# Optimization experiments

Hardware: AMD Instinct MI355X
Metric: run time of the kernel (lower is better)

## Reference

```python
import jax, jax.numpy as jnp
import numpy as np

B, P, C, T, V, H, A = 256, 620, 512, 32, 140, 256, 256


def setup_inputs() -> dict:
    key = jax.random.key(0)
    ks = jax.random.split(key, 8)
    s = lambda k, shape, sc: (jax.random.normal(k, shape, jnp.float32) * sc)
    return {
        "img_features": jax.random.normal(ks[0], (B, P, C), jnp.float32),
        "targets": jax.random.normal(ks[1], (B, T, V), jnp.float32),
        "Ic_w": s(ks[2], (A, C), 0.02), "Ic_b": jnp.zeros((A,), jnp.float32),
        "Hc_w": s(ks[3], (A, H), 0.02), "Hc_b": jnp.zeros((A,), jnp.float32),
        "W_ih": s(ks[4], (4 * H, V + A), 0.02), "W_hh": s(ks[5], (4 * H, H), 0.02),
        "b_ih": jnp.zeros((4 * H,), jnp.float32), "b_hh": jnp.zeros((4 * H,), jnp.float32),
        "Cd_w": s(ks[6], (V, H), 0.02), "Cd_b": jnp.zeros((V,), jnp.float32),
    }


def reference(img_features, targets, Ic_w, Ic_b, Hc_w, Hc_b,
              W_ih, W_hh, b_ih, b_hh, Cd_w, Cd_b):
    # Project image features once: attn_img = Ic(img_features)  [B,P,A]
    attn_img = jnp.einsum('bpc,ac->bpa', img_features, Ic_w) + Ic_b
    scale = 1.0 / jnp.sqrt(jnp.float32(A))
    h0 = jnp.zeros((B, H), jnp.float32)
    c0 = jnp.zeros((B, H), jnp.float32)
    x0 = targets[:, 0, :]  # <start> token logits/one-hot, fed as first rnn input

    def step(carry, _):
        h, c, x = carry
        # attn_hidden = Hc(hidden): [B,A]
        q = h @ Hc_w.T + Hc_b
        # scaled dot-product attention over pixels (keys=values=attn_img)
        w = jax.nn.softmax(jnp.einsum('ba,bpa->bp', q, attn_img) * scale, axis=-1)
        ctx = jnp.einsum('bp,bpa->ba', w, attn_img)  # [B,A]
        # single-step LSTM (PyTorch gate order: i, f, g, o)
        inp = jnp.concatenate([x, ctx], axis=-1)  # [B, V+A]
        gates = inp @ W_ih.T + b_ih + h @ W_hh.T + b_hh
        i, f, g, o = jnp.split(gates, 4, axis=-1)
        c2 = jax.nn.sigmoid(f) * c + jax.nn.sigmoid(i) * jnp.tanh(g)
        h2 = jax.nn.sigmoid(o) * jnp.tanh(c2)
        out = h2 @ Cd_w.T + Cd_b  # [B,V] vocab logits
        # eval path: next rnn_input is the predicted logits
        return (h2, c2, out), out

    _, outs = jax.lax.scan(step, (h0, c0, x0), None, length=T)
    return jnp.transpose(outs, (1, 0, 2))  # [B,T,V]
```

## Files before the change

### kernel.cpp

```cpp
#include <hip/hip_runtime.h>
#include <stdint.h>

#define B_ 256
#define P_ 620
#define C_ 512
#define T_ 32
#define V_ 140
#define H_ 256
#define A_ 256
#define KC 672
#define LOG2E 1.4426950408889634f

typedef unsigned short u16;
typedef __attribute__((ext_vector_type(8))) short bf16x8;
typedef __attribute__((ext_vector_type(4))) float f32x4;

__device__ __forceinline__ float bf2f(u16 u) {
  union { unsigned int i; float f; } v; v.i = ((unsigned int)u) << 16; return v.f;
}
__device__ __forceinline__ float bfu_lo(unsigned int u) {
  union { unsigned int i; float f; } v; v.i = u << 16; return v.f;
}
__device__ __forceinline__ float bfu_hi(unsigned int u) {
  union { unsigned int i; float f; } v; v.i = u & 0xffff0000u; return v.f;
}
__device__ __forceinline__ u16 f2bf(float f) {
  union { float f; unsigned int i; } v; v.f = f;
  unsigned int x = v.i;
  return (u16)((x + 0x7fffu + ((x >> 16) & 1u)) >> 16);
}
__device__ __forceinline__ float sigf(float x) {
  return 1.f / (1.f + __builtin_exp2f(-x * LOG2E));
}
__device__ __forceinline__ float tanhfast(float x) {
  return 1.f - 2.f / (__builtin_exp2f(2.f * LOG2E * x) + 1.f);
}
__device__ __forceinline__ float ld_any(const void* p, size_t idx, int f32) {
  return f32 ? ((const float*)p)[idx] : bf2f(((const u16*)p)[idx]);
}
__device__ __forceinline__ bf16x8 ld8_any(const void* base, size_t off, int f32) {
  if (f32) {
    const float4* p = (const float4*)((const float*)base + off);
    float4 x = p[0], y = p[1];
    bf16x8 r;
    r[0] = (short)f2bf(x.x); r[1] = (short)f2bf(x.y);
    r[2] = (short)f2bf(x.z); r[3] = (short)f2bf(x.w);
    r[4] = (short)f2bf(y.x); r[5] = (short)f2bf(y.y);
    r[6] = (short)f2bf(y.z); r[7] = (short)f2bf(y.w);
    return r;
  }
  return *(const bf16x8*)((const u16*)base + off);
}
__device__ __forceinline__ float dot8(uint4 u, float4 iA, float4 iB) {
  return bfu_lo(u.x) * iA.x + bfu_hi(u.x) * iA.y
       + bfu_lo(u.y) * iA.z + bfu_hi(u.y) * iA.w
       + bfu_lo(u.z) * iB.x + bfu_hi(u.z) * iB.y
       + bfu_lo(u.w) * iB.z + bfu_hi(u.w) * iB.w;
}

__global__ void k_detect(const unsigned int* __restrict__ img, int* __restrict__ flag) {
  __shared__ int mx[256];
  unsigned int u = img[threadIdx.x];
  mx[threadIdx.x] = (int)((u >> 7) & 0xffu);
  __syncthreads();
  if (threadIdx.x == 0) {
    int m = 0;
    #pragma unroll 16
    for (int i = 0; i < 256; i++) m = (mx[i] > m) ? mx[i] : m;
    *flag = (m >= 0x90) ? 1 : 0;
  }
}

__global__ void k_init(const void* __restrict__ W_ih, const void* __restrict__ W_hh,
                       const void* __restrict__ b_ih, const void* __restrict__ b_hh,
                       const void* __restrict__ Hc_w, const void* __restrict__ Hc_b,
                       const void* __restrict__ Cd_w, const void* __restrict__ Cd_b,
                       u16* __restrict__ W_t, float* __restrict__ bias_cat,
                       u16* __restrict__ Hc_wb, float* __restrict__ hcb_f,
                       u16* __restrict__ Cd_wb, float* __restrict__ cdb_f,
                       const int* __restrict__ flag) {
  const int f32 = *flag;
  const int tid = blockIdx.x * blockDim.x + threadIdx.x;
  const int nthr = gridDim.x * blockDim.x;
  for (int idx = tid; idx < 1024 * KC; idx += nthr) {
    int jq = idx / KC, k = idx - jq * KC;
    int j = jq >> 2, q = jq & 3, n = q * H_ + j;
    u16 v = 0;
    if (k < 396) v = f2bf(ld_any(W_ih, (size_t)n * 396 + k, f32));
    else if (k < 652) v = f2bf(ld_any(W_hh, (size_t)n * H_ + (k - 396), f32));
    W_t[(size_t)(k >> 3) * 8192 + jq * 8 + (k & 7)] = v;
  }
  for (int n = tid; n < 1024; n += nthr) {
    int j = n >> 2, q = n & 3, on = q * H_ + j;
    bias_cat[n] = ld_any(b_ih, on, f32) + ld_any(b_hh, on, f32);
  }
  for (int idx = tid; idx < H_ * A_; idx += nthr) Hc_wb[idx] = f2bf(ld_any(Hc_w, idx, f32));
  for (int idx = tid; idx < V_ * H_; idx += nthr) Cd_wb[idx] = f2bf(ld_any(Cd_w, idx, f32));
  for (int n = tid; n < A_; n += nthr) hcb_f[n] = ld_any(Hc_b, n, f32);
  for (int n = tid; n < V_; n += nthr) cdb_f[n] = ld_any(Cd_b, n, f32);
}

__global__ __launch_bounds__(256) void k_proj(const void* __restrict__ img,
                                              const void* __restrict__ Ic_w,
                                              const void* __restrict__ Ic_b,
                                              u16* __restrict__ attn_img,
                                              const int* __restrict__ flag) {
  __shared__ __align__(16) short As[128 * 32];
  __shared__ __align__(16) short Bs[128 * 32];
  const int f32 = *flag;
  const int tid = threadIdx.x;
  const int lane = tid & 63, w = tid >> 6;
  const int wg = blockIdx.x;
  const int m0 = ((wg & 7) + (wg >> 4) * 8) * 128;
  const int n0 = ((wg >> 3) & 1) * 128;
  f32x4 acc[4][4] = {};
  const int wm = w & 1, wn = w >> 1;
  const int fr = lane & 15, fq = lane >> 4;
  const int srow = tid >> 2, scol = (tid & 3) * 8;
  for (int kt = 0; kt < C_; kt += 32) {
    bf16x8 a0 = ld8_any(img, (size_t)(m0 + srow) * C_ + kt + scol, f32);
    bf16x8 a1 = ld8_any(img, (size_t)(m0 + srow + 64) * C_ + kt + scol, f32);
    bf16x8 b0 = ld8_any(Ic_w, (size_t)(n0 + srow) * C_ + kt + scol, f32);
    bf16x8 b1 = ld8_any(Ic_w, (size_t)(n0 + srow + 64) * C_ + kt + scol, f32);
    __syncthreads();
    *(bf16x8*)(As + tid * 8) = a0;
    *(bf16x8*)(As + (tid + 256) * 8) = a1;
    *(bf16x8*)(Bs + tid * 8) = b0;
    *(bf16x8*)(Bs + (tid + 256) * 8) = b1;
    __syncthreads();
    bf16x8 af[4], bfr[4];
    #pragma unroll
    for (int i = 0; i < 4; i++)
      af[i] = *(const bf16x8*)(As + (wm * 64 + i * 16 + fr) * 32 + fq * 8);
    #pragma unroll
    for (int j = 0; j < 4; j++)
      bfr[j] = *(const bf16x8*)(Bs + (wn * 64 + j * 16 + fr) * 32 + fq * 8);
    #pragma unroll
    for (int i = 0; i < 4; i++)
      #pragma unroll
      for (int j = 0; j < 4; j++)
        acc[i][j] = __builtin_amdgcn_mfma_f32_16x16x32_bf16(af[i], bfr[j], acc[i][j], 0, 0, 0);
  }
  #pragma unroll
  for (int i = 0; i < 4; i++) {
    #pragma unroll
    for (int j = 0; j < 4; j++) {
      const int col = n0 + wn * 64 + j * 16 + fr;
      const float bias = ld_any(Ic_b, col, f32);
      #pragma unroll
      for (int rr = 0; rr < 4; rr++) {
        const int row = m0 + wm * 64 + i * 16 + fq * 4 + rr;
        attn_img[(size_t)row * A_ + col] = f2bf(acc[i][j][rr] + bias);
      }
    }
  }
}

__global__ __launch_bounds__(512) void k_seq(
    const u16* __restrict__ Hc_wb, const float* __restrict__ hcb_f,
    const u16* __restrict__ Cd_wb, const float* __restrict__ cdb_f,
    const u16* __restrict__ W_t, const float* __restrict__ bias_cat,
    const u16* __restrict__ attn_img, const void* __restrict__ targets,
    void* __restrict__ d_out, const int* __restrict__ flag) {
  __shared__ float h_s[H_];
  __shared__ float q_s[A_];
  __shared__ __align__(16) float inp_s[KC];
  __shared__ __align__(16) float ctx_s[4][A_];
  __shared__ float red_l[4];
  __shared__ __align__(16) float gpart[1024];
  const int f32 = *flag;
  const int b = blockIdx.x;
  const int tid = threadIdx.x;
  const int lane = tid & 63, w = tid >> 6;

  if (tid < H_) h_s[tid] = 0.f;
  for (int i = tid; i < KC; i += 512) inp_s[i] = 0.f;
  if (tid < V_) inp_s[tid] = ld_any(targets, (size_t)b * T_ * V_ + tid, f32);
  float c_reg = 0.f;
  float4 bias4 = make_float4(0.f, 0.f, 0.f, 0.f);
  if (tid >= 256) bias4 = *(const float4*)(bias_cat + 4 * (tid - 256));
  const float sc = 0.0625f * LOG2E;
  __syncthreads();

  for (int t = 0; t < T_; t++) {
    if (tid < A_) {
      float acc = hcb_f[tid];
      const uint2* wr = (const uint2*)(Hc_wb + tid * H_);
      #pragma unroll 8
      for (int j = 0; j < H_ / 4; j++) {
        uint2 u = wr[j];
        acc += bfu_lo(u.x) * h_s[4 * j] + bfu_hi(u.x) * h_s[4 * j + 1]
             + bfu_lo(u.y) * h_s[4 * j + 2] + bfu_hi(u.y) * h_s[4 * j + 3];
      }
      q_s[tid] = acc;
    } else if (t > 0 && tid < A_ + V_) {
      const int v = tid - A_;
      float acc = cdb_f[v];
      const uint2* wr = (const uint2*)(Cd_wb + v * H_);
      #pragma unroll 8
      for (int j = 0; j < H_ / 4; j++) {
        uint2 u = wr[j];
        acc += bfu_lo(u.x) * h_s[4 * j] + bfu_hi(u.x) * h_s[4 * j + 1]
             + bfu_lo(u.y) * h_s[4 * j + 2] + bfu_hi(u.y) * h_s[4 * j + 3];
      }
      const size_t oo = (size_t)b * T_ * V_ + (size_t)(t - 1) * V_ + v;
      if (f32) ((float*)d_out)[oo] = acc;
      else ((u16*)d_out)[oo] = f2bf(acc);
      inp_s[v] = acc;
    }
    __syncthreads();

    if (w < 4) {
      const int l16 = lane & 15, g = lane >> 4;
      float qr[16];
      #pragma unroll
      for (int e = 0; e < 8; e++) {
        qr[e] = q_s[l16 * 8 + e];
        qr[8 + e] = q_s[128 + l16 * 8 + e];
      }
      const uint4* ap = (const uint4*)(attn_img + (size_t)b * P_ * A_);
      const int pbase = w * 4 + g;
      float l_acc = 0.f;
      float cx[16] = {};
      #pragma unroll 3
      for (int it = 0; it < 39; it++) {
        const int p = pbase + it * 16;
        const int pc = (p < P_) ? p : (P_ - 1);
        const uint4 u0 = ap[(size_t)pc * 32 + l16];
        const uint4 u1 = ap[(size_t)pc * 32 + 16 + l16];
        float v[16];
        v[0] = bfu_lo(u0.x); v[1] = bfu_hi(u0.x);
        v[2] = bfu_lo(u0.y); v[3] = bfu_hi(u0.y);
        v[4] = bfu_lo(u0.z); v[5] = bfu_hi(u0.z);
        v[6] = bfu_lo(u0.w); v[7] = bfu_hi(u0.w);
        v[8] = bfu_lo(u1.x); v[9] = bfu_hi(u1.x);
        v[10] = bfu_lo(u1.y); v[11] = bfu_hi(u1.y);
        v[12] = bfu_lo(u1.z); v[13] = bfu_hi(u1.z);
        v[14] = bfu_lo(u1.w); v[15] = bfu_hi(u1.w);
        float s0 = qr[0] * v[0] + qr[1] * v[1] + qr[2] * v[2] + qr[3] * v[3];
        float s1 = qr[4] * v[4] + qr[5] * v[5] + qr[6] * v[6] + qr[7] * v[7];
        float s2 = qr[8] * v[8] + qr[9] * v[9] + qr[10] * v[10] + qr[11] * v[11];
        float s3 = qr[12] * v[12] + qr[13] * v[13] + qr[14] * v[14] + qr[15] * v[15];
        float s = (s0 + s1) + (s2 + s3);
        s += __shfl_xor(s, 1); s += __shfl_xor(s, 2);
        s += __shfl_xor(s, 4); s += __shfl_xor(s, 8);
        const float sl = (p < P_) ? s * sc : -3.0e38f;
        const float es = __builtin_exp2f(sl - 16.f);
        l_acc += es;
        #pragma unroll
        for (int k = 0; k < 16; k++) cx[k] += es * v[k];
      }
      #pragma unroll
      for (int k = 0; k < 16; k++) {
        cx[k] += __shfl_xor(cx[k], 16);
        cx[k] += __shfl_xor(cx[k], 32);
      }
      l_acc += __shfl_xor(l_acc, 16);
      l_acc += __shfl_xor(l_acc, 32);
      if (g == 0) {
        #pragma unroll
        for (int e = 0; e < 8; e++) {
          ctx_s[w][l16 * 8 + e] = cx[e];
          ctx_s[w][128 + l16 * 8 + e] = cx[8 + e];
        }
        if (l16 == 0) red_l[w] = l_acc;
      }
    } else {
      const int r = tid - 256;
      const uint4* wt4 = (const uint4*)W_t + 4 * r;
      float g0 = bias4.x, g1 = bias4.y, g2 = bias4.z, g3 = bias4.w;
      #pragma unroll 2
      for (int kk = 0; kk < 17; kk++) {
        const float4 iA = *(const float4*)(inp_s + kk * 8);
        const float4 iB = *(const float4*)(inp_s + kk * 8 + 4);
        const uint4 u0 = wt4[kk * 1024 + 0];
        const uint4 u1 = wt4[kk * 1024 + 1];
        const uint4 u2 = wt4[kk * 1024 + 2];
        const uint4 u3 = wt4[kk * 1024 + 3];
        g0 += dot8(u0, iA, iB); g1 += dot8(u1, iA, iB);
        g2 += dot8(u2, iA, iB); g3 += dot8(u3, iA, iB);
      }
      #pragma unroll 2
      for (int kk = 50; kk < 84; kk++) {
        const float4 iA = *(const float4*)(inp_s + kk * 8);
        const float4 iB = *(const float4*)(inp_s + kk * 8 + 4);
        const uint4 u0 = wt4[kk * 1024 + 0];
        const uint4 u1 = wt4[kk * 1024 + 1];
        const uint4 u2 = wt4[kk * 1024 + 2];
        const uint4 u3 = wt4[kk * 1024 + 3];
        g0 += dot8(u0, iA, iB); g1 += dot8(u1, iA, iB);
        g2 += dot8(u2, iA, iB); g3 += dot8(u3, iA, iB);
      }
      gpart[4 * r + 0] = g0; gpart[4 * r + 1] = g1;
      gpart[4 * r + 2] = g2; gpart[4 * r + 3] = g3;
    }
    __syncthreads();

    if (tid < A_) {
      const float l = red_l[0] + red_l[1] + red_l[2] + red_l[3];
      const float cv = ctx_s[0][tid] + ctx_s[1][tid] + ctx_s[2][tid] + ctx_s[3][tid];
      inp_s[V_ + tid] = cv / l;
    }
    __syncthreads();

    {
      const int r2 = tid << 1;
      float g0 = gpart[r2], g1 = gpart[r2 + 1];
      const uint4* wt2 = (const uint4*)W_t + r2;
      #pragma unroll 2
      for (int kk = 17; kk < 50; kk++) {
        const float4 iA = *(const float4*)(inp_s + kk * 8);
        const float4 iB = *(const float4*)(inp_s + kk * 8 + 4);
        const uint4 u0 = wt2[kk * 1024];
        const uint4 u1 = wt2[kk * 1024 + 1];
        g0 += dot8(u0, iA, iB);
        g1 += dot8(u1, iA, iB);
      }
      gpart[r2] = g0; gpart[r2 + 1] = g1;
    }
    __syncthreads();

    if (tid < H_) {
      const float4 g4 = *(const float4*)(gpart + 4 * tid);
      const float is = sigf(g4.x), fs = sigf(g4.y);
      const float gt = tanhfast(g4.z), os = sigf(g4.w);
      const float cn = fs * c_reg + is * gt;
      const float h2 = os * tanhfast(cn);
      c_reg = cn;
      h_s[tid] = h2;
      inp_s[V_ + A_ + tid] = h2;
    }
    __syncthreads();
  }

  if (tid < V_) {
    float acc = cdb_f[tid];
    const uint2* wr = (const uint2*)(Cd_wb + tid * H_);
    #pragma unroll 8
    for (int j = 0; j < H_ / 4; j++) {
      uint2 u = wr[j];
      acc += bfu_lo(u.x) * h_s[4 * j] + bfu_hi(u.x) * h_s[4 * j + 1]
           + bfu_lo(u.y) * h_s[4 * j + 2] + bfu_hi(u.y) * h_s[4 * j + 3];
    }
    const size_t oo = (size_t)b * T_ * V_ + (size_t)(T_ - 1) * V_ + tid;
    if (f32) ((float*)d_out)[oo] = acc;
    else ((u16*)d_out)[oo] = f2bf(acc);
  }
}

extern "C" void kernel_launch(void* const* d_in, const int* in_sizes, int n_in,
                              void* d_out, int out_size, void* d_ws, size_t ws_size,
                              hipStream_t stream) {
  (void)in_sizes; (void)n_in; (void)out_size; (void)ws_size;
  const void* img  = d_in[0];
  const void* tgt  = d_in[1];
  const void* Ic_w = d_in[2];
  const void* Ic_b = d_in[3];
  const void* Hc_w = d_in[4];
  const void* Hc_b = d_in[5];
  const void* W_ih = d_in[6];
  const void* W_hh = d_in[7];
  const void* b_ih = d_in[8];
  const void* b_hh = d_in[9];
  const void* Cd_w = d_in[10];
  const void* Cd_b = d_in[11];

  char* ws = (char*)d_ws;
  size_t off = 0;
  auto alloc = [&](size_t bytes) -> void* {
    void* p = ws + off;
    off += (bytes + 255) & ~(size_t)255;
    return p;
  };
  u16*   attn_img = (u16*)alloc((size_t)B_ * P_ * A_ * 2);
  u16*   W_t      = (u16*)alloc((size_t)1024 * KC * 2);
  float* bias_cat = (float*)alloc(1024 * 4);
  u16*   Hc_wb    = (u16*)alloc((size_t)H_ * A_ * 2);
  float* hcb_f    = (float*)alloc(A_ * 4);
  u16*   Cd_wb    = (u16*)alloc((size_t)V_ * H_ * 2);
  float* cdb_f    = (float*)alloc(V_ * 4);
  int*   flag     = (int*)alloc(256);

  k_detect<<<dim3(1), dim3(256), 0, stream>>>((const unsigned int*)img, flag);
  k_init<<<dim3(512), dim3(256), 0, stream>>>(W_ih, W_hh, b_ih, b_hh,
                                              Hc_w, Hc_b, Cd_w, Cd_b,
                                              W_t, bias_cat,
                                              Hc_wb, hcb_f, Cd_wb, cdb_f, flag);
  k_proj<<<dim3(2480), dim3(256), 0, stream>>>(img, Ic_w, Ic_b, attn_img, flag);
  k_seq<<<dim3(B_), dim3(512), 0, stream>>>(Hc_wb, hcb_f, Cd_wb, cdb_f,
                                            W_t, bias_cat, attn_img, tgt, d_out, flag);
}
```

Measured before the change: 1.912 ms.

## Coalesce weight layouts and software-prefetch loads in sequential LSTM kernel

Repacks the gate weight matrix, Hc and Cd weights so that adjacent threads read adjacent words, making the per-step matvec loads coalesced rather than strided per thread. Adds explicit register double-buffering (prefetch distance 1-2) in the attention loop and the gate matvec loops to hide global-load latency. Sets launch bounds to two blocks per CU, which limits registers while the prefetch buffers add register pressure.

```diff
diff --git a/kernel.cpp b/kernel.cpp
--- a/kernel.cpp
+++ b/kernel.cpp
@@ -75,9 +75,9 @@
                        const void* __restrict__ b_ih, const void* __restrict__ b_hh,
                        const void* __restrict__ Hc_w, const void* __restrict__ Hc_b,
                        const void* __restrict__ Cd_w, const void* __restrict__ Cd_b,
-                       u16* __restrict__ W_t, float* __restrict__ bias_cat,
-                       u16* __restrict__ Hc_wb, float* __restrict__ hcb_f,
-                       u16* __restrict__ Cd_wb, float* __restrict__ cdb_f,
+                       u16* __restrict__ W2, float* __restrict__ bias_cat,
+                       unsigned int* __restrict__ Hc_p, float* __restrict__ hcb_f,
+                       unsigned int* __restrict__ Cd_p, float* __restrict__ cdb_f,
                        const int* __restrict__ flag) {
   const int f32 = *flag;
   const int tid = blockIdx.x * blockDim.x + threadIdx.x;
@@ -88,14 +88,25 @@
     u16 v = 0;
     if (k < 396) v = f2bf(ld_any(W_ih, (size_t)n * 396 + k, f32));
     else if (k < 652) v = f2bf(ld_any(W_hh, (size_t)n * H_ + (k - 396), f32));
-    W_t[(size_t)(k >> 3) * 8192 + jq * 8 + (k & 7)] = v;
+    const int kk = k >> 3, e = k & 7, blk = jq >> 8, r = jq & 255;
+    W2[((size_t)(kk * 4 + blk) * 256 + r) * 8 + e] = v;
   }
   for (int n = tid; n < 1024; n += nthr) {
     int j = n >> 2, q = n & 3, on = q * H_ + j;
     bias_cat[n] = ld_any(b_ih, on, f32) + ld_any(b_hh, on, f32);
   }
-  for (int idx = tid; idx < H_ * A_; idx += nthr) Hc_wb[idx] = f2bf(ld_any(Hc_w, idx, f32));
-  for (int idx = tid; idx < V_ * H_; idx += nthr) Cd_wb[idx] = f2bf(ld_any(Cd_w, idx, f32));
+  for (int idx = tid; idx < 128 * 256; idx += nthr) {
+    int j2 = idx >> 8, n = idx & 255;
+    u16 lo = f2bf(ld_any(Hc_w, (size_t)n * H_ + 2 * j2, f32));
+    u16 hi = f2bf(ld_any(Hc_w, (size_t)n * H_ + 2 * j2 + 1, f32));
+    Hc_p[idx] = (unsigned int)lo | ((unsigned int)hi << 16);
+  }
+  for (int idx = tid; idx < 128 * 140; idx += nthr) {
+    int j2 = idx / 140, v = idx - j2 * 140;
+    u16 lo = f2bf(ld_any(Cd_w, (size_t)v * H_ + 2 * j2, f32));
+    u16 hi = f2bf(ld_any(Cd_w, (size_t)v * H_ + 2 * j2 + 1, f32));
+    Cd_p[idx] = (unsigned int)lo | ((unsigned int)hi << 16);
+  }
   for (int n = tid; n < A_; n += nthr) hcb_f[n] = ld_any(Hc_b, n, f32);
   for (int n = tid; n < V_; n += nthr) cdb_f[n] = ld_any(Cd_b, n, f32);
 }
@@ -156,10 +167,10 @@
   }
 }
 
-__global__ __launch_bounds__(512) void k_seq(
-    const u16* __restrict__ Hc_wb, const float* __restrict__ hcb_f,
-    const u16* __restrict__ Cd_wb, const float* __restrict__ cdb_f,
-    const u16* __restrict__ W_t, const float* __restrict__ bias_cat,
+__global__ __launch_bounds__(512, 2) void k_seq(
+    const unsigned int* __restrict__ Hc_p, const float* __restrict__ hcb_f,
+    const unsigned int* __restrict__ Cd_p, const float* __restrict__ cdb_f,
+    const u16* __restrict__ W2, const float* __restrict__ bias_cat,
     const u16* __restrict__ attn_img, const void* __restrict__ targets,
     void* __restrict__ d_out, const int* __restrict__ flag) {
   __shared__ float h_s[H_];
@@ -172,36 +183,37 @@
   const int b = blockIdx.x;
   const int tid = threadIdx.x;
   const int lane = tid & 63, w = tid >> 6;
+  const uint4* wb = (const uint4*)W2;
 
   if (tid < H_) h_s[tid] = 0.f;
   for (int i = tid; i < KC; i += 512) inp_s[i] = 0.f;
   if (tid < V_) inp_s[tid] = ld_any(targets, (size_t)b * T_ * V_ + tid, f32);
   float c_reg = 0.f;
-  float4 bias4 = make_float4(0.f, 0.f, 0.f, 0.f);
-  if (tid >= 256) bias4 = *(const float4*)(bias_cat + 4 * (tid - 256));
+  float bias_b0 = 0.f, bias_b1 = 0.f, bias_b2 = 0.f, bias_b3 = 0.f;
+  if (tid >= 256) {
+    const int r = tid - 256;
+    bias_b0 = bias_cat[r];       bias_b1 = bias_cat[256 + r];
+    bias_b2 = bias_cat[512 + r]; bias_b3 = bias_cat[768 + r];
+  }
   const float sc = 0.0625f * LOG2E;
   __syncthreads();
 
   for (int t = 0; t < T_; t++) {
     if (tid < A_) {
       float acc = hcb_f[tid];
-      const uint2* wr = (const uint2*)(Hc_wb + tid * H_);
       #pragma unroll 8
-      for (int j = 0; j < H_ / 4; j++) {
-        uint2 u = wr[j];
-        acc += bfu_lo(u.x) * h_s[4 * j] + bfu_hi(u.x) * h_s[4 * j + 1]
-             + bfu_lo(u.y) * h_s[4 * j + 2] + bfu_hi(u.y) * h_s[4 * j + 3];
+      for (int j2 = 0; j2 < H_ / 2; j2++) {
+        const unsigned int u = Hc_p[j2 * 256 + tid];
+        acc += bfu_lo(u) * h_s[2 * j2] + bfu_hi(u) * h_s[2 * j2 + 1];
       }
       q_s[tid] = acc;
     } else if (t > 0 && tid < A_ + V_) {
       const int v = tid - A_;
       float acc = cdb_f[v];
-      const uint2* wr = (const uint2*)(Cd_wb + v * H_);
       #pragma unroll 8
-      for (int j = 0; j < H_ / 4; j++) {
-        uint2 u = wr[j];
-        acc += bfu_lo(u.x) * h_s[4 * j] + bfu_hi(u.x) * h_s[4 * j + 1]
-             + bfu_lo(u.y) * h_s[4 * j + 2] + bfu_hi(u.y) * h_s[4 * j + 3];
+      for (int j2 = 0; j2 < H_ / 2; j2++) {
+        const unsigned int u = Cd_p[j2 * 140 + v];
+        acc += bfu_lo(u) * h_s[2 * j2] + bfu_hi(u) * h_s[2 * j2 + 1];
       }
       const size_t oo = (size_t)b * T_ * V_ + (size_t)(t - 1) * V_ + v;
       if (f32) ((float*)d_out)[oo] = acc;
@@ -220,23 +232,27 @@
       }
       const uint4* ap = (const uint4*)(attn_img + (size_t)b * P_ * A_);
       const int pbase = w * 4 + g;
+      uint4 cu0 = ap[(size_t)pbase * 32 + l16];
+      uint4 cu1 = ap[(size_t)pbase * 32 + 16 + l16];
+      uint4 nu0 = ap[(size_t)(pbase + 16) * 32 + l16];
+      uint4 nu1 = ap[(size_t)(pbase + 16) * 32 + 16 + l16];
       float l_acc = 0.f;
       float cx[16] = {};
-      #pragma unroll 3
       for (int it = 0; it < 39; it++) {
+        int pf = pbase + (it + 2) * 16;
+        pf = (pf < P_) ? pf : (P_ - 1);
+        const uint4 fu0 = ap[(size_t)pf * 32 + l16];
+        const uint4 fu1 = ap[(size_t)pf * 32 + 16 + l16];
         const int p = pbase + it * 16;
-        const int pc = (p < P_) ? p : (P_ - 1);
-        const uint4 u0 = ap[(size_t)pc * 32 + l16];
-        const uint4 u1 = ap[(size_t)pc * 32 + 16 + l16];
         float v[16];
-        v[0] = bfu_lo(u0.x); v[1] = bfu_hi(u0.x);
-        v[2] = bfu_lo(u0.y); v[3] = bfu_hi(u0.y);
-        v[4] = bfu_lo(u0.z); v[5] = bfu_hi(u0.z);
-        v[6] = bfu_lo(u0.w); v[7] = bfu_hi(u0.w);
-        v[8] = bfu_lo(u1.x); v[9] = bfu_hi(u1.x);
-        v[10] = bfu_lo(u1.y); v[11] = bfu_hi(u1.y);
-        v[12] = bfu_lo(u1.z); v[13] = bfu_hi(u1.z);
-        v[14] = bfu_lo(u1.w); v[15] = bfu_hi(u1.w);
+        v[0] = bfu_lo(cu0.x); v[1] = bfu_hi(cu0.x);
+        v[2] = bfu_lo(cu0.y); v[3] = bfu_hi(cu0.y);
+        v[4] = bfu_lo(cu0.z); v[5] = bfu_hi(cu0.z);
+        v[6] = bfu_lo(cu0.w); v[7] = bfu_hi(cu0.w);
+        v[8] = bfu_lo(cu1.x); v[9] = bfu_hi(cu1.x);
+        v[10] = bfu_lo(cu1.y); v[11] = bfu_hi(cu1.y);
+        v[12] = bfu_lo(cu1.z); v[13] = bfu_hi(cu1.z);
+        v[14] = bfu_lo(cu1.w); v[15] = bfu_hi(cu1.w);
         float s0 = qr[0] * v[0] + qr[1] * v[1] + qr[2] * v[2] + qr[3] * v[3];
         float s1 = qr[4] * v[4] + qr[5] * v[5] + qr[6] * v[6] + qr[7] * v[7];
         float s2 = qr[8] * v[8] + qr[9] * v[9] + qr[10] * v[10] + qr[11] * v[11];
@@ -249,6 +265,7 @@
         l_acc += es;
         #pragma unroll
         for (int k = 0; k < 16; k++) cx[k] += es * v[k];
+        cu0 = nu0; cu1 = nu1; nu0 = fu0; nu1 = fu1;
       }
       #pragma unroll
       for (int k = 0; k < 16; k++) {
@@ -267,32 +284,28 @@
       }
     } else {
       const int r = tid - 256;
-      const uint4* wt4 = (const uint4*)W_t + 4 * r;
-      float g0 = bias4.x, g1 = bias4.y, g2 = bias4.z, g3 = bias4.w;
-      #pragma unroll 2
-      for (int kk = 0; kk < 17; kk++) {
+      float g0 = bias_b0, g1 = bias_b1, g2 = bias_b2, g3 = bias_b3;
+      int kk = 0;
+      uint4 a0 = wb[(0 * 4 + 0) * 256 + r];
+      uint4 a1 = wb[(0 * 4 + 1) * 256 + r];
+      uint4 a2 = wb[(0 * 4 + 2) * 256 + r];
+      uint4 a3 = wb[(0 * 4 + 3) * 256 + r];
+      #pragma unroll 3
+      for (int i = 0; i < 51; i++) {
+        const int ni = (i + 1 < 51) ? i + 1 : 50;
+        const int nk = ni + ((ni >= 17) ? 33 : 0);
+        const uint4 b0v = wb[(nk * 4 + 0) * 256 + r];
+        const uint4 b1v = wb[(nk * 4 + 1) * 256 + r];
+        const uint4 b2v = wb[(nk * 4 + 2) * 256 + r];
+        const uint4 b3v = wb[(nk * 4 + 3) * 256 + r];
         const float4 iA = *(const float4*)(inp_s + kk * 8);
         const float4 iB = *(const float4*)(inp_s + kk * 8 + 4);
-        const uint4 u0 = wt4[kk * 1024 + 0];
-        const uint4 u1 = wt4[kk * 1024 + 1];
-        const uint4 u2 = wt4[kk * 1024 + 2];
-        const uint4 u3 = wt4[kk * 1024 + 3];
-        g0 += dot8(u0, iA, iB); g1 += dot8(u1, iA, iB);
-        g2 += dot8(u2, iA, iB); g3 += dot8(u3, iA, iB);
-      }
-      #pragma unroll 2
-      for (int kk = 50; kk < 84; kk++) {
-        const float4 iA = *(const float4*)(inp_s + kk * 8);
-        const float4 iB = *(const float4*)(inp_s + kk * 8 + 4);
-        const uint4 u0 = wt4[kk * 1024 + 0];
-        const uint4 u1 = wt4[kk * 1024 + 1];
-        const uint4 u2 = wt4[kk * 1024 + 2];
-        const uint4 u3 = wt4[kk * 1024 + 3];
-        g0 += dot8(u0, iA, iB); g1 += dot8(u1, iA, iB);
-        g2 += dot8(u2, iA, iB); g3 += dot8(u3, iA, iB);
-      }
-      gpart[4 * r + 0] = g0; gpart[4 * r + 1] = g1;
-      gpart[4 * r + 2] = g2; gpart[4 * r + 3] = g3;
+        g0 += dot8(a0, iA, iB); g1 += dot8(a1, iA, iB);
+        g2 += dot8(a2, iA, iB); g3 += dot8(a3, iA, iB);
+        a0 = b0v; a1 = b1v; a2 = b2v; a3 = b3v; kk = nk;
+      }
+      gpart[r] = g0; gpart[256 + r] = g1;
+      gpart[512 + r] = g2; gpart[768 + r] = g3;
     }
     __syncthreads();
 
@@ -304,19 +317,22 @@
     __syncthreads();
 
     {
-      const int r2 = tid << 1;
-      float g0 = gpart[r2], g1 = gpart[r2 + 1];
-      const uint4* wt2 = (const uint4*)W_t + r2;
-      #pragma unroll 2
+      float g0 = gpart[tid], g1 = gpart[tid + 512];
+      const int blo = tid >> 8, rr = tid & 255;
+      uint4 a0 = wb[(17 * 4 + blo) * 256 + rr];
+      uint4 a1 = wb[(17 * 4 + 2 + blo) * 256 + rr];
+      #pragma unroll 4
       for (int kk = 17; kk < 50; kk++) {
+        const int nk = (kk + 1 < 50) ? kk + 1 : 49;
+        const uint4 b0v = wb[(nk * 4 + blo) * 256 + rr];
+        const uint4 b1v = wb[(nk * 4 + 2 + blo) * 256 + rr];
         const float4 iA = *(const float4*)(inp_s + kk * 8);
         const float4 iB = *(const float4*)(inp_s + kk * 8 + 4);
-        const uint4 u0 = wt2[kk * 1024];
-        const uint4 u1 = wt2[kk * 1024 + 1];
-        g0 += dot8(u0, iA, iB);
-        g1 += dot8(u1, iA, iB);
-      }
-      gpart[r2] = g0; gpart[r2 + 1] = g1;
+        g0 += dot8(a0, iA, iB);
+        g1 += dot8(a1, iA, iB);
+        a0 = b0v; a1 = b1v;
+      }
+      gpart[tid] = g0; gpart[tid + 512] = g1;
     }
     __syncthreads();
 
@@ -335,12 +351,10 @@
 
   if (tid < V_) {
     float acc = cdb_f[tid];
-    const uint2* wr = (const uint2*)(Cd_wb + tid * H_);
     #pragma unroll 8
-    for (int j = 0; j < H_ / 4; j++) {
-      uint2 u = wr[j];
-      acc += bfu_lo(u.x) * h_s[4 * j] + bfu_hi(u.x) * h_s[4 * j + 1]
-           + bfu_lo(u.y) * h_s[4 * j + 2] + bfu_hi(u.y) * h_s[4 * j + 3];
+    for (int j2 = 0; j2 < H_ / 2; j2++) {
+      const unsigned int u = Cd_p[j2 * 140 + tid];
+      acc += bfu_lo(u) * h_s[2 * j2] + bfu_hi(u) * h_s[2 * j2 + 1];
     }
     const size_t oo = (size_t)b * T_ * V_ + (size_t)(T_ - 1) * V_ + tid;
     if (f32) ((float*)d_out)[oo] = acc;
@@ -373,20 +387,20 @@
     return p;
   };
   u16*   attn_img = (u16*)alloc((size_t)B_ * P_ * A_ * 2);
-  u16*   W_t      = (u16*)alloc((size_t)1024 * KC * 2);
+  u16*   W2       = (u16*)alloc((size_t)1024 * KC * 2);
   float* bias_cat = (float*)alloc(1024 * 4);
-  u16*   Hc_wb    = (u16*)alloc((size_t)H_ * A_ * 2);
+  unsigned int* Hc_p = (unsigned int*)alloc((size_t)128 * 256 * 4);
   float* hcb_f    = (float*)alloc(A_ * 4);
-  u16*   Cd_wb    = (u16*)alloc((size_t)V_ * H_ * 2);
+  unsigned int* Cd_p = (unsigned int*)alloc((size_t)128 * 140 * 4);
   float* cdb_f    = (float*)alloc(V_ * 4);
   int*   flag     = (int*)alloc(256);
 
   k_detect<<<dim3(1), dim3(256), 0, stream>>>((const unsigned int*)img, flag);
   k_init<<<dim3(512), dim3(256), 0, stream>>>(W_ih, W_hh, b_ih, b_hh,
                                               Hc_w, Hc_b, Cd_w, Cd_b,
-                                              W_t, bias_cat,
-                                              Hc_wb, hcb_f, Cd_wb, cdb_f, flag);
+                                              W2, bias_cat,
+                                              Hc_p, hcb_f, Cd_p, cdb_f, flag);
   k_proj<<<dim3(2480), dim3(256), 0, stream>>>(img, Ic_w, Ic_b, attn_img, flag);
-  k_seq<<<dim3(B_), dim3(512), 0, stream>>>(Hc_wb, hcb_f, Cd_wb, cdb_f,
-                                            W_t, bias_cat, attn_img, tgt, d_out, flag);
-}
+  k_seq<<<dim3(B_), dim3(512), 0, stream>>>(Hc_p, hcb_f, Cd_p, cdb_f,
+                                            W2, bias_cat, attn_img, tgt, d_out, flag);
+}
```

New measurement: 1.730 ms. -9.5%, faster.
